# Optimization experiments

Measured on AMD Instinct MI355X. Metric: run time of the kernel, lower is better.

Reference implementation:

```python
import jax, jax.numpy as jnp
import numpy as np

LAMBDA = 10.0      # sinkhorn_lambda from init_kwargs
N_ITERS = 100      # fixed Sinkhorn iteration count
B, T_MAX, D_MAX = 256, 256, 256
TP, DP = T_MAX + 1, D_MAX + 1   # expanded with births/deaths row+col
L = TP * DP                      # padded flat output length per example
EPS = 1e-12


def setup_inputs() -> dict:
    key = jax.random.key(0)
    k1, k2, k3 = jax.random.split(key, 3)
    affinity_scores = jax.random.uniform(k1, (B, T_MAX, D_MAX), dtype=jnp.float32)
    num_detections = jax.random.randint(k2, (B,), 32, D_MAX + 1, dtype=jnp.int32)
    num_tracklets = jax.random.randint(k3, (B,), 32, T_MAX + 1, dtype=jnp.int32)
    return {
        "affinity_scores": affinity_scores,
        "num_detections": num_detections,
        "num_tracklets": num_tracklets,
    }


def _sinkhorn_transport(aff, nd, nt):
    """Masked Sinkhorn on the expanded (nt+1)x(nd+1) matrix, padded to [TP,DP]."""
    r = jnp.arange(TP)
    c = jnp.arange(DP)
    row_valid = r <= nt          # nt tracklet rows + 1 births/deaths row
    col_valid = c <= nd
    interior = (r[:, None] < nt) & (c[None, :] < nd)
    aff_pad = jnp.pad(aff, ((0, 1), (0, 1)))
    aff_e = jnp.where(interior, aff_pad, 0.0)   # dummy row/col have affinity 0
    mask = (row_valid[:, None] & col_valid[None, :]).astype(aff.dtype)
    # cost = -affinity  =>  kernel K = exp(-lambda * cost) = exp(lambda * affinity)
    K = jnp.exp(LAMBDA * aff_e) * mask
    ndf = nd.astype(aff.dtype)
    ntf = nt.astype(aff.dtype)
    # target marginals: [1,...,1, length] on valid entries, 0 on padding
    row_sums = jnp.where(r < nt, 1.0, jnp.where(r == nt, ndf, 0.0))
    col_sums = jnp.where(c < nd, 1.0, jnp.where(c == nd, ntf, 0.0))
    u0 = jnp.zeros((TP,), aff.dtype)
    v0 = col_valid.astype(aff.dtype)

    def body(carry, _):
        u, v = carry
        u = jnp.where(row_valid, row_sums / (K @ v + EPS), 0.0)
        v = jnp.where(col_valid, col_sums / (K.T @ u + EPS), 0.0)
        return (u, v), None

    (u, v), _ = jax.lax.scan(body, (u0, v0), None, length=N_ITERS)
    transport = u[:, None] * K * v[None, :]
    return transport, interior, row_valid, col_valid


def _single(aff, nd, nt):
    transport, interior, row_valid, col_valid = _sinkhorn_transport(aff, nd, nt)
    r = jnp.arange(TP)
    c = jnp.arange(DP)

    # hard assignment on transport[:-1,:-1] (valid interior): mutual argmax
    neg_inf = jnp.array(-jnp.inf, transport.dtype)
    t_in = jnp.where(interior, transport, neg_inf)
    row_max = jnp.max(t_in, axis=1, keepdims=True)
    col_max = jnp.max(t_in, axis=0, keepdims=True)
    assign_in = interior & (t_in == row_max) & (t_in == col_max)
    # births/deaths: unmatched tracklets -> death col nd; unmatched detections -> birth row nt
    row_has = jnp.any(assign_in, axis=1)
    col_has = jnp.any(assign_in, axis=0)
    deaths = (r[:, None] < nt) & (c[None, :] == nd) & (~row_has)[:, None]
    births = (r[:, None] == nt) & (c[None, :] < nd) & (~col_has)[None, :]
    assignment = assign_in | deaths | births

    # flatten the (nt+1)x(nd+1) valid submatrix row-major, zero-pad to length L
    k = jnp.arange(L)
    length = (nt + 1) * (nd + 1)
    rr = jnp.clip(k // (nd + 1), 0, T_MAX)
    cc = k % (nd + 1)
    valid = k < length
    t_flat = jnp.where(valid, transport[rr, cc], 0.0)
    a_flat = jnp.where(valid, assignment[rr, cc], False)
    return t_flat, a_flat


def reference(affinity_scores, num_detections, num_tracklets):
    t_flat, a_flat = jax.vmap(_single)(affinity_scores, num_detections, num_tracklets)
    return t_flat, a_flat
```

## Files before the change

### kernel.cpp

```cpp
#include <hip/hip_runtime.h>


#define T_MAX   256
#define L_FLAT  (257 * 257)
#define N_ITERS 100
#define LAMBDA_F 10.0f
#define EPS_F    1e-12f
#define KTP     264

#define ROR1 0x121
#define ROR2 0x122
#define ROR4 0x124
#define ROR8 0x128

typedef short bf8   __attribute__((ext_vector_type(8)));
typedef float f32x4 __attribute__((ext_vector_type(4)));

template<int CTRL>
__device__ __forceinline__ float dpp_addf(float x) {
    int t = __builtin_amdgcn_update_dpp(0, __float_as_int(x), CTRL, 0xF, 0xF, true);
    return x + __int_as_float(t);
}
__device__ __forceinline__ float swz16_addf(float x) {
    return x + __int_as_float(__builtin_amdgcn_ds_swizzle(__float_as_int(x), 0x401F));
}
__device__ __forceinline__ float swz16_maxf(float x) {
    return fmaxf(x, __int_as_float(__builtin_amdgcn_ds_swizzle(__float_as_int(x), 0x401F)));
}
__device__ __forceinline__ int swz16_ori(int x) {
    return x | __builtin_amdgcn_ds_swizzle(x, 0x401F);
}
__device__ __forceinline__ float fast_rcp(float x) {
#if __has_builtin(__builtin_amdgcn_rcpf)
    return __builtin_amdgcn_rcpf(x);
#else
    return 1.0f / x;
#endif
}
__device__ __forceinline__ unsigned short f2bf(float x) {
    unsigned u = __float_as_uint(x);
    return (unsigned short)((u + 0x7FFFu + ((u >> 16) & 1u)) >> 16);
}
__device__ __forceinline__ float bf2f(short s) {
    return __uint_as_float(((unsigned)(unsigned short)s) << 16);
}

__global__ __launch_bounds__(512, 2) void assoc_sinkhorn_kernel(
    const float* __restrict__ aff,
    const int*   __restrict__ ndet,
    const int*   __restrict__ ntrk,
    float*       __restrict__ out_t,
    float*       __restrict__ out_a)
{
    const int b   = blockIdx.x;
    const int nd  = ndet[b];
    const int nt  = ntrk[b];
    const int tid = threadIdx.x;
    const int w   = tid >> 6;
    const int l   = tid & 63;
    const int lr  = l & 15;
    const int lk  = l >> 4;

    __shared__ __align__(16) unsigned short KT[256 * KTP];
    __shared__ __align__(16) unsigned short u_bf[256];
    __shared__ __align__(16) unsigned short v_bf[256];
    __shared__ __align__(16) float u_f[256];
    __shared__ __align__(16) float v_f[256];
    __shared__ __align__(16) float supart[8];
    __shared__ __align__(16) float svpart[8];
    __shared__ __align__(16) float rm_s[256];
    __shared__ __align__(16) float cm_s[256];

    const float ndf = (float)nd;
    const float ntf = (float)nt;

    bf8 KA[2][8];
    const float* Ab = aff + (size_t)b * (T_MAX * T_MAX);

    #pragma unroll
    for (int a = 0; a < 2; ++a) {
        const int row = 32 * w + 16 * a + lr;
        const bool rv = (row < nt);
        const float* rp = Ab + (size_t)row * T_MAX;
        #pragma unroll
        for (int t = 0; t < 8; ++t) {
            const int c0 = 32 * t + 8 * lk;
            const float4 x0 = *reinterpret_cast<const float4*>(rp + c0);
            const float4 x1 = *reinterpret_cast<const float4*>(rp + c0 + 4);
            const float e[8] = {x0.x, x0.y, x0.z, x0.w, x1.x, x1.y, x1.z, x1.w};
            bf8 kk;
            #pragma unroll
            for (int j = 0; j < 8; ++j) {
                const float val = (rv && (c0 + j) < nd) ? __expf(LAMBDA_F * e[j]) : 0.0f;
                const unsigned short bits = f2bf(val);
                kk[j] = (short)bits;
                KT[(c0 + j) * KTP + row] = bits;
            }
            KA[a][t] = kk;
        }
    }

    if (tid < 256) {
        v_bf[tid] = (tid < nd) ? f2bf(1.0f) : (unsigned short)0;
        v_f[tid]  = (tid < nd) ? 1.0f : 0.0f;
    }
    __syncthreads();

    float Sv  = ndf;
    float vbd = 1.0f;
    float ubd = 0.0f;

    const int r_a0 = 32 * w + 4 * lk;
    const int myc0 = 32 * w + lr;
    const int myc1 = myc0 + 16;
    const unsigned short* KT0 = &KT[myc0 * KTP];
    const unsigned short* KT1 = &KT[myc1 * KTP];

    for (int it = 0; it < N_ITERS; ++it) {
        bf8 VF[8];
        #pragma unroll
        for (int t = 0; t < 8; ++t)
            VF[t] = *reinterpret_cast<const bf8*>(&v_bf[32 * t + 8 * lk]);

        f32x4 acc0 = {0.0f, 0.0f, 0.0f, 0.0f};
        f32x4 acc1 = {0.0f, 0.0f, 0.0f, 0.0f};
        #pragma unroll
        for (int t = 0; t < 8; ++t) {
            acc0 = __builtin_amdgcn_mfma_f32_16x16x32_bf16(KA[0][t], VF[t], acc0, 0, 0, 0);
            acc1 = __builtin_amdgcn_mfma_f32_16x16x32_bf16(KA[1][t], VF[t], acc1, 0, 0, 0);
        }

        const float ubd_new = ndf * fast_rcp(Sv + vbd + EPS_F);
        const float vbdE = vbd + EPS_F;
        float u8[8];
        #pragma unroll
        for (int q = 0; q < 4; ++q) {
            u8[q]     = ((r_a0 + q)      < nt) ? fast_rcp(acc0[q] + vbdE) : 0.0f;
            u8[4 + q] = ((r_a0 + 16 + q) < nt) ? fast_rcp(acc1[q] + vbdE) : 0.0f;
        }

        {
            float su = ((u8[0] + u8[1]) + (u8[2] + u8[3]))
                     + ((u8[4] + u8[5]) + (u8[6] + u8[7]));
            su = swz16_addf(su);
            su += __shfl_xor(su, 32, 64);
            if (l == 0) supart[w] = su;
        }

        if (lr == 0) {
            const unsigned p01 = (unsigned)f2bf(u8[0]) | ((unsigned)f2bf(u8[1]) << 16);
            const unsigned p23 = (unsigned)f2bf(u8[2]) | ((unsigned)f2bf(u8[3]) << 16);
            const unsigned p45 = (unsigned)f2bf(u8[4]) | ((unsigned)f2bf(u8[5]) << 16);
            const unsigned p67 = (unsigned)f2bf(u8[6]) | ((unsigned)f2bf(u8[7]) << 16);
            *reinterpret_cast<uint2*>(&u_bf[r_a0])      = uint2{p01, p23};
            *reinterpret_cast<uint2*>(&u_bf[r_a0 + 16]) = uint2{p45, p67};
            f32x4 uf0 = {u8[0], u8[1], u8[2], u8[3]};
            f32x4 uf1 = {u8[4], u8[5], u8[6], u8[7]};
            *reinterpret_cast<f32x4*>(&u_f[r_a0])      = uf0;
            *reinterpret_cast<f32x4*>(&u_f[r_a0 + 16]) = uf1;
        }
        __syncthreads();

        f32x4 qa0 = {0.0f, 0.0f, 0.0f, 0.0f};
        f32x4 qa1 = {0.0f, 0.0f, 0.0f, 0.0f};
        #pragma unroll
        for (int t = 0; t < 8; ++t) {
            const bf8 UF = *reinterpret_cast<const bf8*>(&u_bf[32 * t + 8 * lk]);
            const bf8 b0 = *reinterpret_cast<const bf8*>(&KT0[32 * t + 8 * lk]);
            const bf8 b1 = *reinterpret_cast<const bf8*>(&KT1[32 * t + 8 * lk]);
            qa0 = __builtin_amdgcn_mfma_f32_16x16x32_bf16(UF, b0, qa0, 0, 0, 0);
            qa1 = __builtin_amdgcn_mfma_f32_16x16x32_bf16(UF, b1, qa1, 0, 0, 0);
        }

        const f32x4 sp0 = *reinterpret_cast<const f32x4*>(&supart[0]);
        const f32x4 sp1 = *reinterpret_cast<const f32x4*>(&supart[4]);
        const float Su = ((sp0[0] + sp0[1]) + (sp0[2] + sp0[3]))
                       + ((sp1[0] + sp1[1]) + (sp1[2] + sp1[3]));
        const float vbd_new = ntf * fast_rcp(Su + ubd_new + EPS_F);

        const float ubdE = ubd_new + EPS_F;
        const float v0 = (myc0 < nd) ? fast_rcp(qa0[0] + ubdE) : 0.0f;
        const float v1 = (myc1 < nd) ? fast_rcp(qa1[0] + ubdE) : 0.0f;

        {
            float sv = v0 + v1;
            sv = dpp_addf<ROR1>(sv);
            sv = dpp_addf<ROR2>(sv);
            sv = dpp_addf<ROR4>(sv);
            sv = dpp_addf<ROR8>(sv);
            if (l == 0) svpart[w] = sv;
        }
        if (lk == 0) {
            v_bf[myc0] = f2bf(v0);
            v_bf[myc1] = f2bf(v1);
            v_f[myc0]  = v0;
            v_f[myc1]  = v1;
        }
        ubd = ubd_new;
        vbd = vbd_new;
        __syncthreads();

        const f32x4 vp0 = *reinterpret_cast<const f32x4*>(&svpart[0]);
        const f32x4 vp1 = *reinterpret_cast<const f32x4*>(&svpart[4]);
        Sv = ((vp0[0] + vp0[1]) + (vp0[2] + vp0[3]))
           + ((vp1[0] + vp1[1]) + (vp1[2] + vp1[3]));
    }

    float rm[2];
    #pragma unroll
    for (int a = 0; a < 2; ++a) {
        const int row = 32 * w + 16 * a + lr;
        const float ur = u_f[row];
        float mm = 0.0f;
        #pragma unroll
        for (int t = 0; t < 8; ++t) {
            const f32x4 va = *reinterpret_cast<const f32x4*>(&v_f[32 * t + 8 * lk]);
            const f32x4 vb = *reinterpret_cast<const f32x4*>(&v_f[32 * t + 8 * lk + 4]);
            const float vj[8] = {va[0], va[1], va[2], va[3], vb[0], vb[1], vb[2], vb[3]};
            #pragma unroll
            for (int j = 0; j < 8; ++j) {
                const float tv = ur * bf2f(KA[a][t][j]) * vj[j];
                mm = fmaxf(mm, tv);
            }
        }
        mm = swz16_maxf(mm);
        mm = fmaxf(mm, __shfl_xor(mm, 32, 64));
        rm[a] = mm;
        if (lk == 0) rm_s[row] = mm;
    }
    float cmv[2];
    #pragma unroll
    for (int c = 0; c < 2; ++c) {
        const int col = (c == 0) ? myc0 : myc1;
        const unsigned short* KTc = (c == 0) ? KT0 : KT1;
        const float vc = v_f[col];
        float mm = 0.0f;
        #pragma unroll
        for (int t = 0; t < 8; ++t) {
            const int rb = 32 * t + 8 * lk;
            const bf8 kb = *reinterpret_cast<const bf8*>(&KTc[rb]);
            const f32x4 ua = *reinterpret_cast<const f32x4*>(&u_f[rb]);
            const f32x4 ub = *reinterpret_cast<const f32x4*>(&u_f[rb + 4]);
            const float uj[8] = {ua[0], ua[1], ua[2], ua[3], ub[0], ub[1], ub[2], ub[3]};
            #pragma unroll
            for (int j = 0; j < 8; ++j) {
                const float tv = uj[j] * bf2f(kb[j]) * vc;
                mm = fmaxf(mm, tv);
            }
        }
        mm = swz16_maxf(mm);
        mm = fmaxf(mm, __shfl_xor(mm, 32, 64));
        cmv[c] = mm;
        if (lk == 0) cm_s[col] = mm;
    }
    __syncthreads();

    float* Ot = out_t + (size_t)b * L_FLAT;
    float* Oa = out_a + (size_t)b * L_FLAT;
    const int stride = nd + 1;

    #pragma unroll
    for (int c = 0; c < 2; ++c) {
        const int col = (c == 0) ? myc0 : myc1;
        const unsigned short* KTc = (c == 0) ? KT0 : KT1;
        const float vc = v_f[col];
        const float cmc = cmv[c];
        const bool cv = (col < nd);
        int has = 0;
        #pragma unroll
        for (int t = 0; t < 8; ++t) {
            const int rb = 32 * t + 8 * lk;
            const bf8 kb = *reinterpret_cast<const bf8*>(&KTc[rb]);
            const f32x4 ua = *reinterpret_cast<const f32x4*>(&u_f[rb]);
            const f32x4 ub = *reinterpret_cast<const f32x4*>(&u_f[rb + 4]);
            const f32x4 ra = *reinterpret_cast<const f32x4*>(&rm_s[rb]);
            const f32x4 rb4 = *reinterpret_cast<const f32x4*>(&rm_s[rb + 4]);
            const float uj[8] = {ua[0], ua[1], ua[2], ua[3], ub[0], ub[1], ub[2], ub[3]};
            const float rj[8] = {ra[0], ra[1], ra[2], ra[3], rb4[0], rb4[1], rb4[2], rb4[3]};
            #pragma unroll
            for (int j = 0; j < 8; ++j) {
                const int rowj = rb + j;
                const float tv = uj[j] * bf2f(kb[j]) * vc;
                const bool bit = (rowj < nt) && cv && (tv == rj[j]) && (tv == cmc);
                has |= bit ? 1 : 0;
            }
        }
        has = swz16_ori(has);
        has |= __shfl_xor(has, 32, 64);
        if (lk == 0 && cv) {
            const int kk = nt * stride + col;
            Ot[kk] = ubd * vc;
            Oa[kk] = has ? 0.0f : 1.0f;
        }
    }
    if (tid == 0) {
        const int kk = nt * stride + nd;
        Ot[kk] = ubd * vbd;
        Oa[kk] = 0.0f;
    }

    #pragma unroll
    for (int a = 0; a < 2; ++a) {
        const int row = 32 * w + 16 * a + lr;
        const float ur = u_f[row];
        const float rma = rm[a];
        const bool rv = (row < nt);
        int has = 0;
        #pragma unroll
        for (int t = 0; t < 8; ++t) {
            const int cb = 32 * t + 8 * lk;
            const f32x4 va  = *reinterpret_cast<const f32x4*>(&v_f[cb]);
            const f32x4 vb  = *reinterpret_cast<const f32x4*>(&v_f[cb + 4]);
            const f32x4 ca  = *reinterpret_cast<const f32x4*>(&cm_s[cb]);
            const f32x4 cb4 = *reinterpret_cast<const f32x4*>(&cm_s[cb + 4]);
            const float vj[8] = {va[0], va[1], va[2], va[3], vb[0], vb[1], vb[2], vb[3]};
            const float cj[8] = {ca[0], ca[1], ca[2], ca[3], cb4[0], cb4[1], cb4[2], cb4[3]};
            #pragma unroll
            for (int j = 0; j < 8; ++j) {
                const int colj = cb + j;
                const float tv = ur * bf2f(KA[a][t][j]) * vj[j];
                const bool bit = rv && (colj < nd) && (tv == rma) && (tv == cj[j]);
                has |= bit ? 1 : 0;
                if (rv && colj < nd) {
                    Ot[row * stride + colj] = tv;
                    Oa[row * stride + colj] = bit ? 1.0f : 0.0f;
                }
            }
        }
        has = swz16_ori(has);
        has |= __shfl_xor(has, 32, 64);
        if (lk == 0 && rv) {
            const int kk = row * stride + nd;
            Ot[kk] = ur * vbd;
            Oa[kk] = has ? 0.0f : 1.0f;
        }
    }

    const int length = (nt + 1) * stride;
    for (int k = length + tid; k < L_FLAT; k += 512) {
        Ot[k] = 0.0f;
        Oa[k] = 0.0f;
    }
}

extern "C" void kernel_launch(void* const* d_in, const int* in_sizes, int n_in,
                              void* d_out, int out_size, void* d_ws, size_t ws_size,
                              hipStream_t stream)
{
    const float* aff  = (const float*)d_in[0];
    const int*   ndet = (const int*)d_in[1];
    const int*   ntrk = (const int*)d_in[2];
    const int    Bn   = in_sizes[1];
    float* out_t = (float*)d_out;
    float* out_a = out_t + (size_t)Bn * L_FLAT;
    assoc_sinkhorn_kernel<<<dim3(Bn), dim3(512), 0, stream>>>(aff, ndet, ntrk, out_t, out_a);
}
```

Baseline: 423.3 us.

## Hold transposed K tile in registers instead of LDS and vectorize output stores

```diff
diff --git a/kernel.cpp b/kernel.cpp
--- a/kernel.cpp
+++ b/kernel.cpp
@@ -6,7 +6,6 @@
 #define N_ITERS 100
 #define LAMBDA_F 10.0f
 #define EPS_F    1e-12f
-#define KTP     264
 
 #define ROR1 0x121
 #define ROR2 0x122
@@ -15,6 +14,8 @@
 
 typedef short bf8   __attribute__((ext_vector_type(8)));
 typedef float f32x4 __attribute__((ext_vector_type(4)));
+
+struct F4 { float a, b, c, d; };
 
 template<int CTRL>
 __device__ __forceinline__ float dpp_addf(float x) {
@@ -45,7 +46,7 @@
     return __uint_as_float(((unsigned)(unsigned short)s) << 16);
 }
 
-__global__ __launch_bounds__(512, 2) void assoc_sinkhorn_kernel(
+__global__ __launch_bounds__(512, 1) void assoc_sinkhorn_kernel(
     const float* __restrict__ aff,
     const int*   __restrict__ ndet,
     const int*   __restrict__ ntrk,
@@ -61,7 +62,6 @@
     const int lr  = l & 15;
     const int lk  = l >> 4;
 
-    __shared__ __align__(16) unsigned short KT[256 * KTP];
     __shared__ __align__(16) unsigned short u_bf[256];
     __shared__ __align__(16) unsigned short v_bf[256];
     __shared__ __align__(16) float u_f[256];
@@ -75,6 +75,7 @@
     const float ntf = (float)nt;
 
     bf8 KA[2][8];
+    bf8 KB[2][8];
     const float* Ab = aff + (size_t)b * (T_MAX * T_MAX);
 
     #pragma unroll
@@ -92,11 +93,26 @@
             #pragma unroll
             for (int j = 0; j < 8; ++j) {
                 const float val = (rv && (c0 + j) < nd) ? __expf(LAMBDA_F * e[j]) : 0.0f;
-                const unsigned short bits = f2bf(val);
-                kk[j] = (short)bits;
-                KT[(c0 + j) * KTP + row] = bits;
+                kk[j] = (short)f2bf(val);
             }
             KA[a][t] = kk;
+        }
+    }
+    #pragma unroll
+    for (int c = 0; c < 2; ++c) {
+        const int col = 32 * w + 16 * c + lr;
+        const bool cv = (col < nd);
+        #pragma unroll
+        for (int t = 0; t < 8; ++t) {
+            const int r0 = 32 * t + 8 * lk;
+            bf8 kk;
+            #pragma unroll
+            for (int j = 0; j < 8; ++j) {
+                const float x = Ab[(size_t)(r0 + j) * T_MAX + col];
+                const float val = (cv && (r0 + j) < nt) ? __expf(LAMBDA_F * x) : 0.0f;
+                kk[j] = (short)f2bf(val);
+            }
+            KB[c][t] = kk;
         }
     }
 
@@ -113,8 +129,6 @@
     const int r_a0 = 32 * w + 4 * lk;
     const int myc0 = 32 * w + lr;
     const int myc1 = myc0 + 16;
-    const unsigned short* KT0 = &KT[myc0 * KTP];
-    const unsigned short* KT1 = &KT[myc1 * KTP];
 
     for (int it = 0; it < N_ITERS; ++it) {
         bf8 VF[8];
@@ -166,10 +180,8 @@
         #pragma unroll
         for (int t = 0; t < 8; ++t) {
             const bf8 UF = *reinterpret_cast<const bf8*>(&u_bf[32 * t + 8 * lk]);
-            const bf8 b0 = *reinterpret_cast<const bf8*>(&KT0[32 * t + 8 * lk]);
-            const bf8 b1 = *reinterpret_cast<const bf8*>(&KT1[32 * t + 8 * lk]);
-            qa0 = __builtin_amdgcn_mfma_f32_16x16x32_bf16(UF, b0, qa0, 0, 0, 0);
-            qa1 = __builtin_amdgcn_mfma_f32_16x16x32_bf16(UF, b1, qa1, 0, 0, 0);
+            qa0 = __builtin_amdgcn_mfma_f32_16x16x32_bf16(UF, KB[0][t], qa0, 0, 0, 0);
+            qa1 = __builtin_amdgcn_mfma_f32_16x16x32_bf16(UF, KB[1][t], qa1, 0, 0, 0);
         }
 
         const f32x4 sp0 = *reinterpret_cast<const f32x4*>(&supart[0]);
@@ -232,19 +244,18 @@
     #pragma unroll
     for (int c = 0; c < 2; ++c) {
         const int col = (c == 0) ? myc0 : myc1;
-        const unsigned short* KTc = (c == 0) ? KT0 : KT1;
         const float vc = v_f[col];
         float mm = 0.0f;
         #pragma unroll
         for (int t = 0; t < 8; ++t) {
             const int rb = 32 * t + 8 * lk;
-            const bf8 kb = *reinterpret_cast<const bf8*>(&KTc[rb]);
             const f32x4 ua = *reinterpret_cast<const f32x4*>(&u_f[rb]);
             const f32x4 ub = *reinterpret_cast<const f32x4*>(&u_f[rb + 4]);
             const float uj[8] = {ua[0], ua[1], ua[2], ua[3], ub[0], ub[1], ub[2], ub[3]};
             #pragma unroll
             for (int j = 0; j < 8; ++j) {
-                const float tv = uj[j] * bf2f(kb[j]) * vc;
+                const float kv = (c == 0) ? bf2f(KB[0][t][j]) : bf2f(KB[1][t][j]);
+                const float tv = uj[j] * kv * vc;
                 mm = fmaxf(mm, tv);
             }
         }
@@ -262,7 +273,6 @@
     #pragma unroll
     for (int c = 0; c < 2; ++c) {
         const int col = (c == 0) ? myc0 : myc1;
-        const unsigned short* KTc = (c == 0) ? KT0 : KT1;
         const float vc = v_f[col];
         const float cmc = cmv[c];
         const bool cv = (col < nd);
@@ -270,7 +280,6 @@
         #pragma unroll
         for (int t = 0; t < 8; ++t) {
             const int rb = 32 * t + 8 * lk;
-            const bf8 kb = *reinterpret_cast<const bf8*>(&KTc[rb]);
             const f32x4 ua = *reinterpret_cast<const f32x4*>(&u_f[rb]);
             const f32x4 ub = *reinterpret_cast<const f32x4*>(&u_f[rb + 4]);
             const f32x4 ra = *reinterpret_cast<const f32x4*>(&rm_s[rb]);
@@ -280,7 +289,8 @@
             #pragma unroll
             for (int j = 0; j < 8; ++j) {
                 const int rowj = rb + j;
-                const float tv = uj[j] * bf2f(kb[j]) * vc;
+                const float kv = (c == 0) ? bf2f(KB[0][t][j]) : bf2f(KB[1][t][j]);
+                const float tv = uj[j] * kv * vc;
                 const bool bit = (rowj < nt) && cv && (tv == rj[j]) && (tv == cmc);
                 has |= bit ? 1 : 0;
             }
@@ -313,17 +323,42 @@
             const f32x4 vb  = *reinterpret_cast<const f32x4*>(&v_f[cb + 4]);
             const f32x4 ca  = *reinterpret_cast<const f32x4*>(&cm_s[cb]);
             const f32x4 cb4 = *reinterpret_cast<const f32x4*>(&cm_s[cb + 4]);
-            const float vj[8] = {va[0], va[1], va[2], va[3], vb[0], vb[1], vb[2], vb[3]};
-            const float cj[8] = {ca[0], ca[1], ca[2], ca[3], cb4[0], cb4[1], cb4[2], cb4[3]};
-            #pragma unroll
-            for (int j = 0; j < 8; ++j) {
-                const int colj = cb + j;
-                const float tv = ur * bf2f(KA[a][t][j]) * vj[j];
-                const bool bit = rv && (colj < nd) && (tv == rma) && (tv == cj[j]);
+            float tvs[8];
+            float abs_[8];
+            #pragma unroll
+            for (int j = 0; j < 4; ++j) {
+                const float tv = ur * bf2f(KA[a][t][j]) * va[j];
+                const bool bit = rv && ((cb + j) < nd) && (tv == rma) && (tv == ca[j]);
+                tvs[j] = tv; abs_[j] = bit ? 1.0f : 0.0f;
                 has |= bit ? 1 : 0;
-                if (rv && colj < nd) {
-                    Ot[row * stride + colj] = tv;
-                    Oa[row * stride + colj] = bit ? 1.0f : 0.0f;
+            }
+            #pragma unroll
+            for (int j = 0; j < 4; ++j) {
+                const float tv = ur * bf2f(KA[a][t][4 + j]) * vb[j];
+                const bool bit = rv && ((cb + 4 + j) < nd) && (tv == rma) && (tv == cb4[j]);
+                tvs[4 + j] = tv; abs_[4 + j] = bit ? 1.0f : 0.0f;
+                has |= bit ? 1 : 0;
+            }
+            if (rv) {
+                float* OtR = Ot + (size_t)row * stride;
+                float* OaR = Oa + (size_t)row * stride;
+                #pragma unroll
+                for (int g = 0; g < 2; ++g) {
+                    const int c0 = cb + 4 * g;
+                    if (c0 + 3 < nd) {
+                        F4 ot = {tvs[4*g], tvs[4*g+1], tvs[4*g+2], tvs[4*g+3]};
+                        F4 oa = {abs_[4*g], abs_[4*g+1], abs_[4*g+2], abs_[4*g+3]};
+                        *reinterpret_cast<F4*>(OtR + c0) = ot;
+                        *reinterpret_cast<F4*>(OaR + c0) = oa;
+                    } else {
+                        #pragma unroll
+                        for (int j = 0; j < 4; ++j) {
+                            if (c0 + j < nd) {
+                                OtR[c0 + j] = tvs[4*g + j];
+                                OaR[c0 + j] = abs_[4*g + j];
+                            }
+                        }
+                    }
                 }
             }
         }
```

Result: slower. 561.4 us (+32.6%).
